# Kernel tuning notes

Measured on AMD Instinct MI355X. Metric: run time of the kernel, lower is better.

The kernel has to match this reference:

```python
import jax, jax.numpy as jnp
import numpy as np

D_MODEL = 256
D_FFN = 1024
N_LEVELS = 4
N_HEADS = 8
N_POINTS = 4
HEAD_DIM = D_MODEL // N_HEADS
SPATIAL = [(128, 128), (64, 64), (32, 32), (16, 16)]
LQ = sum(h * w for h, w in SPATIAL)  # 21760
B = 2


def setup_inputs() -> dict:
    key = jax.random.key(0)
    ks = jax.random.split(key, 24)

    def w(k, shape, s=0.02):
        return (jax.random.normal(k, shape) * s).astype(jnp.float32)

    HLP = N_HEADS * N_LEVELS * N_POINTS
    starts = np.cumsum([0] + [h * w_ for h, w_ in SPATIAL[:-1]])
    return {
        "src": jax.random.normal(ks[0], (B, LQ, D_MODEL), jnp.float32),
        "pos": 0.1 * jax.random.normal(ks[1], (B, LQ, D_MODEL), jnp.float32),
        "reference_points": jax.random.uniform(ks[2], (B, LQ, N_LEVELS, 2), jnp.float32),
        "W_off": w(ks[3], (D_MODEL, HLP * 2)),
        "b_off": w(ks[4], (HLP * 2,), 0.5),
        "W_attn": w(ks[5], (D_MODEL, HLP)),
        "b_attn": jnp.zeros((HLP,), jnp.float32),
        "W_val": w(ks[6], (D_MODEL, D_MODEL)),
        "b_val": jnp.zeros((D_MODEL,), jnp.float32),
        "W_out": w(ks[7], (D_MODEL, D_MODEL)),
        "b_out": jnp.zeros((D_MODEL,), jnp.float32),
        "ln1_g": jnp.ones((D_MODEL,), jnp.float32),
        "ln1_b": jnp.zeros((D_MODEL,), jnp.float32),
        "W1": w(ks[8], (D_MODEL, D_FFN)),
        "b1": jnp.zeros((D_FFN,), jnp.float32),
        "W2": w(ks[9], (D_FFN, D_MODEL)),
        "b2": jnp.zeros((D_MODEL,), jnp.float32),
        "ln2_g": jnp.ones((D_MODEL,), jnp.float32),
        "ln2_b": jnp.zeros((D_MODEL,), jnp.float32),
        "spatial_shapes": np.array(SPATIAL, np.int32),
        "level_start_index": np.array(starts, np.int32),
    }


def _layernorm(x, g, b):
    mu = x.mean(-1, keepdims=True)
    var = ((x - mu) ** 2).mean(-1, keepdims=True)
    return (x - mu) * jax.lax.rsqrt(var + 1e-5) * g + b


def _bilinear_sample(v, x, y, H, W):
    # v: [N, H, W, D]; x, y: [N, Lq, P] pixel coords (align_corners=False, zero pad)
    x0f = jnp.floor(x)
    y0f = jnp.floor(y)
    x0 = x0f.astype(jnp.int32)
    y0 = y0f.astype(jnp.int32)
    wx1 = x - x0f
    wy1 = y - y0f
    wx0 = 1.0 - wx1
    wy0 = 1.0 - wy1
    vf = v.reshape(v.shape[0], H * W, v.shape[-1])

    def gather(xi, yi, wt):
        valid = (xi >= 0) & (xi < W) & (yi >= 0) & (yi < H)
        idx = jnp.clip(yi, 0, H - 1) * W + jnp.clip(xi, 0, W - 1)
        g = jnp.take_along_axis(vf, idx.reshape(idx.shape[0], -1)[..., None], axis=1)
        g = g.reshape(*xi.shape, vf.shape[-1])
        return g * (wt * valid.astype(wt.dtype))[..., None]

    return (gather(x0, y0, wx0 * wy0) + gather(x0 + 1, y0, wx1 * wy0)
            + gather(x0, y0 + 1, wx0 * wy1) + gather(x0 + 1, y0 + 1, wx1 * wy1))


def _ms_deform_attn(query, src, reference_points, W_off, b_off, W_attn, b_attn,
                    W_val, b_val, W_out, b_out, spatial_shapes):
    Bq, Lq, _ = query.shape
    ss = np.asarray(spatial_shapes)
    value = (src @ W_val + b_val).reshape(Bq, Lq, N_HEADS, HEAD_DIM)
    off = (query @ W_off + b_off).reshape(Bq, Lq, N_HEADS, N_LEVELS, N_POINTS, 2)
    attn = (query @ W_attn + b_attn).reshape(Bq, Lq, N_HEADS, N_LEVELS * N_POINTS)
    attn = jax.nn.softmax(attn, axis=-1).reshape(Bq, Lq, N_HEADS, N_LEVELS, N_POINTS)
    # offset normalizer = (W, H) per level
    normalizer = jnp.asarray(ss[:, ::-1].astype(np.float32))  # [L, 2]
    loc = reference_points[:, :, None, :, None, :] + off / normalizer[None, None, None, :, None, :]
    # loc: [B, Lq, M, L, P, 2] normalized in [0,1]
    out = jnp.zeros((Bq, N_HEADS, Lq, HEAD_DIM), query.dtype)
    start = 0
    for lvl in range(N_LEVELS):
        H, W = int(ss[lvl, 0]), int(ss[lvl, 1])
        v = value[:, start:start + H * W]                                 # [B, HW, M, D]
        v = v.transpose(0, 2, 1, 3).reshape(Bq * N_HEADS, H, W, HEAD_DIM)
        l = loc[:, :, :, lvl]                                             # [B, Lq, M, P, 2]
        x = (l[..., 0] * W - 0.5).transpose(0, 2, 1, 3).reshape(Bq * N_HEADS, Lq, N_POINTS)
        y = (l[..., 1] * H - 0.5).transpose(0, 2, 1, 3).reshape(Bq * N_HEADS, Lq, N_POINTS)
        sampled = _bilinear_sample(v, x, y, H, W)                         # [BM, Lq, P, D]
        wgt = attn[:, :, :, lvl].transpose(0, 2, 1, 3).reshape(Bq * N_HEADS, Lq, N_POINTS)
        out = out + (sampled * wgt[..., None]).sum(2).reshape(Bq, N_HEADS, Lq, HEAD_DIM)
        start += H * W
    out = out.transpose(0, 2, 1, 3).reshape(Bq, Lq, D_MODEL)
    return out @ W_out + b_out


def reference(src, pos, reference_points, W_off, b_off, W_attn, b_attn, W_val, b_val,
              W_out, b_out, ln1_g, ln1_b, W1, b1, W2, b2, ln2_g, ln2_b,
              spatial_shapes, level_start_index):
    query = src + pos
    src2 = _ms_deform_attn(query, src, reference_points, W_off, b_off, W_attn, b_attn,
                           W_val, b_val, W_out, b_out, spatial_shapes)
    h = _layernorm(src + src2, ln1_g, ln1_b)
    ffn = jax.nn.relu(h @ W1 + b1) @ W2 + b2
    return _layernorm(h + ffn, ln2_g, ln2_b)
```

## Files before the change

kernel.cpp:

```cpp
#include <hip/hip_runtime.h>

typedef __bf16 bf16x8 __attribute__((ext_vector_type(8)));
typedef float f32x4 __attribute__((ext_vector_type(4)));

static constexpr int TOKS = 43520;
static constexpr int LQN  = 21760;

__device__ __forceinline__ unsigned short f2bf(float f) {
  union { float f; unsigned u; } v; v.f = f;
  return (unsigned short)((v.u + 0x7fffu + ((v.u >> 16) & 1u)) >> 16);
}
__device__ __forceinline__ float bf2f(unsigned short b) {
  union { unsigned u; float f; } v; v.u = ((unsigned)b) << 16; return v.f;
}

__global__ __launch_bounds__(256) void prewt_kernel(
    const float* __restrict__ src, const float* __restrict__ pos,
    unsigned short* __restrict__ srcb, unsigned short* __restrict__ qb,
    const float* __restrict__ W_val, const float* __restrict__ W_off,
    const float* __restrict__ W_attn, const float* __restrict__ W_out,
    const float* __restrict__ W1, const float* __restrict__ W2,
    const float* __restrict__ b_off, const float* __restrict__ b_attn,
    unsigned short* __restrict__ Wt_val, unsigned short* __restrict__ Wt_oa,
    unsigned short* __restrict__ Wt_out,
    unsigned short* __restrict__ Wt_1, unsigned short* __restrict__ Wt_2,
    float* __restrict__ b_oa) {
  const int bid = blockIdx.x;
  if (bid < 10880) {
    int i = bid * 256 + threadIdx.x;
    float4 s = ((const float4*)src)[i], p = ((const float4*)pos)[i];
    ((ushort4*)srcb)[i] = make_ushort4(f2bf(s.x), f2bf(s.y), f2bf(s.z), f2bf(s.w));
    ((ushort4*)qb)[i]   = make_ushort4(f2bf(s.x + p.x), f2bf(s.y + p.y),
                                       f2bf(s.z + p.z), f2bf(s.w + p.w));
    return;
  }
  int gid = (bid - 10880) * 256 + threadIdx.x;
  if (gid >= 754048) return;
  if (gid >= 753664) {
    int i = gid - 753664;
    b_oa[i] = (i < 256) ? b_off[i] : b_attn[i - 256];
    return;
  }
  const float* W; unsigned short* Wt; int idx, K, nsh;
  if (gid < 65536)       { W = W_val;  Wt = Wt_val;          idx = gid;          K = 256;  nsh = 8;  }
  else if (gid < 131072) { W = W_off;  Wt = Wt_oa;           idx = gid - 65536;  K = 256;  nsh = 8;  }
  else if (gid < 163840) { W = W_attn; Wt = Wt_oa + 65536;   idx = gid - 131072; K = 256;  nsh = 7;  }
  else if (gid < 229376) { W = W_out;  Wt = Wt_out;          idx = gid - 163840; K = 256;  nsh = 8;  }
  else if (gid < 491520) { W = W1;     Wt = Wt_1;            idx = gid - 229376; K = 256;  nsh = 10; }
  else                   { W = W2;     Wt = Wt_2;            idx = gid - 491520; K = 1024; nsh = 8;  }
  int k = idx >> nsh, n = idx & ((1 << nsh) - 1);
  Wt[n * K + k] = f2bf(W[idx]);
}

template <int K, int OUTOP>
__device__ __forceinline__ void gemm_body(unsigned short* __restrict__ As,
                                          unsigned short* __restrict__ Bs,
                                          const unsigned short* __restrict__ A,
                                          const unsigned short* __restrict__ Bt,
                                          const float* __restrict__ bias,
                                          const unsigned short* __restrict__ res,
                                          unsigned short* __restrict__ Cp,
                                          int N, int bm, int bn) {
  const int t = threadIdx.x;
  const int wave = t >> 6, lane = t & 63;
  const int wm = (wave & 1) << 6, wn = (wave >> 1) << 6;
  const int lr = lane & 15, lq = lane >> 4;
  const int row0 = t >> 2, cb0 = (t & 3) << 3;
  f32x4 acc[4][4] = {};
  const unsigned short* ga = A  + (size_t)(bm * 128 + row0) * K + cb0;
  const unsigned short* gb = Bt + (size_t)(bn * 128 + row0) * K + cb0;
  const size_t gs = (size_t)64 * K;
  uint4 pa0 = *(const uint4*)ga;
  uint4 pa1 = *(const uint4*)(ga + gs);
  uint4 pb0 = *(const uint4*)gb;
  uint4 pb1 = *(const uint4*)(gb + gs);
  int p = 0;
#pragma unroll 1
  for (int k0 = 0; k0 < K; k0 += 32) {
    unsigned short* Ab = As + p * 5120;
    unsigned short* Bb = Bs + p * 5120;
    *(uint4*)&Ab[row0 * 40 + cb0] = pa0;
    *(uint4*)&Ab[(row0 + 64) * 40 + cb0] = pa1;
    *(uint4*)&Bb[row0 * 40 + cb0] = pb0;
    *(uint4*)&Bb[(row0 + 64) * 40 + cb0] = pb1;
    __syncthreads();
    if (k0 + 32 < K) {
      pa0 = *(const uint4*)(ga + k0 + 32);
      pa1 = *(const uint4*)(ga + gs + k0 + 32);
      pb0 = *(const uint4*)(gb + k0 + 32);
      pb1 = *(const uint4*)(gb + gs + k0 + 32);
    }
    bf16x8 af[4], bfr[4];
#pragma unroll
    for (int i = 0; i < 4; i++) af[i] = *(const bf16x8*)&Ab[(wm + i * 16 + lr) * 40 + lq * 8];
#pragma unroll
    for (int j = 0; j < 4; j++) bfr[j] = *(const bf16x8*)&Bb[(wn + j * 16 + lr) * 40 + lq * 8];
#pragma unroll
    for (int i = 0; i < 4; i++)
#pragma unroll
      for (int j = 0; j < 4; j++)
        acc[i][j] = __builtin_amdgcn_mfma_f32_16x16x32_bf16(af[i], bfr[j], acc[i][j], 0, 0, 0);
    p ^= 1;
  }
  const int rb = bm * 128 + wm + lq * 4;
  const int cbase = bn * 128 + wn + lr;
#pragma unroll
  for (int j = 0; j < 4; j++) {
    const int col = cbase + j * 16;
    const float bv = bias[col];
#pragma unroll
    for (int i = 0; i < 4; i++) {
#pragma unroll
      for (int r = 0; r < 4; r++) {
        float v = acc[i][j][r] + bv;
        size_t o = (size_t)(rb + i * 16 + r) * N + col;
        if (OUTOP == 1) Cp[o] = f2bf(v);
        else if (OUTOP == 2) Cp[o] = f2bf(fmaxf(v, 0.f));
        else Cp[o] = f2bf(v + bf2f(res[o]));
      }
    }
  }
}

__global__ __launch_bounds__(256) void proj_kernel(
    const unsigned short* __restrict__ srcb, const unsigned short* __restrict__ qb,
    const unsigned short* __restrict__ Wt_val, const unsigned short* __restrict__ Wt_oa,
    const float* __restrict__ b_val, const float* __restrict__ b_oa,
    unsigned short* __restrict__ valb, unsigned short* __restrict__ oab) {
  __shared__ unsigned short As[2 * 5120];
  __shared__ unsigned short Bs[2 * 5120];
  const int bn = blockIdx.y;
  if (bn < 2)
    gemm_body<256, 1>(As, Bs, srcb, Wt_val, b_val, nullptr, valb, 256, blockIdx.x, bn);
  else
    gemm_body<256, 1>(As, Bs, qb, Wt_oa, b_oa, nullptr, oab, 384, blockIdx.x, bn - 2);
}

__global__ __launch_bounds__(256, 2) void fused_tail_kernel(
    const unsigned short* __restrict__ attn,
    const unsigned short* __restrict__ Wot,
    const float* __restrict__ b_out,
    const unsigned short* __restrict__ srcres,
    const float* __restrict__ g1, const float* __restrict__ be1,
    const unsigned short* __restrict__ W1t,
    const unsigned short* __restrict__ W2t,
    const float* __restrict__ b1, const float* __restrict__ b2,
    const float* __restrict__ g2, const float* __restrict__ be2,
    float* __restrict__ out) {
  __shared__ unsigned short Ah[64 * 264];
  __shared__ unsigned short Hc[64 * 136];
  __shared__ float red[2][4][64];
  const int t = threadIdx.x;
  const int w = t >> 6, lane = t & 63;
  const int lr = lane & 15, lq = lane >> 4;
  const size_t rowbase = (size_t)blockIdx.x * 64;

  {
    const uint4* gsrc = (const uint4*)(attn + rowbase * 256);
#pragma unroll
    for (int u = 0; u < 8; u++) {
      const int idx = u * 256 + t;
      const int row = idx >> 5, c8 = idx & 31;
      *(uint4*)&Ah[row * 264 + c8 * 8] = gsrc[idx];
    }
  }
  __syncthreads();

  f32x4 acc0[4][4] = {};
  {
    const size_t wb = (size_t)(w * 64 + lr) * 256;
    bf16x8 pf0 = *(const bf16x8*)&Wot[wb + lq * 8];
    bf16x8 pf1 = *(const bf16x8*)&Wot[wb + 16 * 256 + lq * 8];
    bf16x8 pf2 = *(const bf16x8*)&Wot[wb + 32 * 256 + lq * 8];
    bf16x8 pf3 = *(const bf16x8*)&Wot[wb + 48 * 256 + lq * 8];
#pragma unroll 1
    for (int ks = 0; ks < 8; ks++) {
      const int k0 = ks * 32;
      bf16x8 c0 = pf0, c1 = pf1, c2 = pf2, c3 = pf3;
      if (ks < 7) {
        pf0 = *(const bf16x8*)&Wot[wb + k0 + 32 + lq * 8];
        pf1 = *(const bf16x8*)&Wot[wb + 16 * 256 + k0 + 32 + lq * 8];
        pf2 = *(const bf16x8*)&Wot[wb + 32 * 256 + k0 + 32 + lq * 8];
        pf3 = *(const bf16x8*)&Wot[wb + 48 * 256 + k0 + 32 + lq * 8];
      }
      bf16x8 af[4];
#pragma unroll
      for (int i = 0; i < 4; i++)
        af[i] = *(const bf16x8*)&Ah[(i * 16 + lr) * 264 + k0 + lq * 8];
#pragma unroll
      for (int i = 0; i < 4; i++) {
        acc0[i][0] = __builtin_amdgcn_mfma_f32_16x16x32_bf16(af[i], c0, acc0[i][0], 0, 0, 0);
        acc0[i][1] = __builtin_amdgcn_mfma_f32_16x16x32_bf16(af[i], c1, acc0[i][1], 0, 0, 0);
        acc0[i][2] = __builtin_amdgcn_mfma_f32_16x16x32_bf16(af[i], c2, acc0[i][2], 0, 0, 0);
        acc0[i][3] = __builtin_amdgcn_mfma_f32_16x16x32_bf16(af[i], c3, acc0[i][3], 0, 0, 0);
      }
    }
  }
  {
    float vsum[4][4], vsq[4][4];
#pragma unroll
    for (int i = 0; i < 4; i++)
#pragma unroll
      for (int r = 0; r < 4; r++) { vsum[i][r] = 0.f; vsq[i][r] = 0.f; }
#pragma unroll
    for (int j = 0; j < 4; j++) {
      const int col = w * 64 + j * 16 + lr;
      const float bv = b_out[col];
#pragma unroll
      for (int i = 0; i < 4; i++)
#pragma unroll
        for (int r = 0; r < 4; r++) {
          const int row = i * 16 + lq * 4 + r;
          float v = acc0[i][j][r] + bv + bf2f(srcres[(rowbase + row) * 256 + col]);
          acc0[i][j][r] = v;
          vsum[i][r] += v;
          vsq[i][r]  += v * v;
        }
    }
#pragma unroll
    for (int m = 1; m <= 8; m <<= 1)
#pragma unroll
      for (int i = 0; i < 4; i++)
#pragma unroll
        for (int r = 0; r < 4; r++) {
          vsum[i][r] += __shfl_xor(vsum[i][r], m, 64);
          vsq[i][r]  += __shfl_xor(vsq[i][r],  m, 64);
        }
    if (lr == 0) {
#pragma unroll
      for (int i = 0; i < 4; i++)
#pragma unroll
        for (int r = 0; r < 4; r++) {
          const int row = i * 16 + lq * 4 + r;
          red[0][w][row] = vsum[i][r];
          red[1][w][row] = vsq[i][r];
        }
    }
    __syncthreads();
    float mu[4][4], rstd[4][4];
#pragma unroll
    for (int i = 0; i < 4; i++)
#pragma unroll
      for (int r = 0; r < 4; r++) {
        const int row = i * 16 + lq * 4 + r;
        const float ts = red[0][0][row] + red[0][1][row] + red[0][2][row] + red[0][3][row];
        const float tq = red[1][0][row] + red[1][1][row] + red[1][2][row] + red[1][3][row];
        const float m_ = ts * (1.f / 256.f);
        mu[i][r] = m_;
        rstd[i][r] = rsqrtf(tq * (1.f / 256.f) - m_ * m_ + 1e-5f);
      }
#pragma unroll
    for (int j = 0; j < 4; j++) {
      const int col = w * 64 + j * 16 + lr;
      const float gg = g1[col], bb = be1[col];
#pragma unroll
      for (int i = 0; i < 4; i++)
#pragma unroll
        for (int r = 0; r < 4; r++) {
          const int row = i * 16 + lq * 4 + r;
          const float y = (acc0[i][j][r] - mu[i][r]) * rstd[i][r] * gg + bb;
          Ah[row * 264 + col] = f2bf(y);
        }
    }
  }
  __syncthreads();

  f32x4 acc2[4][4] = {};
  const int c1base = w * 32;
#pragma unroll 1
  for (int c2 = 0; c2 < 8; c2++) {
    f32x4 acc1[4][2] = {};
    const size_t w1r0 = (size_t)(c2 * 128 + c1base + lr) * 256;
    const size_t w1r1 = (size_t)(c2 * 128 + c1base + 16 + lr) * 256;
    bf16x8 bfn0 = *(const bf16x8*)&W1t[w1r0 + lq * 8];
    bf16x8 bfn1 = *(const bf16x8*)&W1t[w1r1 + lq * 8];
#pragma unroll 1
    for (int ks = 0; ks < 8; ks++) {
      const int k0 = ks * 32;
      bf16x8 b0 = bfn0, b1v = bfn1;
      if (ks < 7) {
        bfn0 = *(const bf16x8*)&W1t[w1r0 + k0 + 32 + lq * 8];
        bfn1 = *(const bf16x8*)&W1t[w1r1 + k0 + 32 + lq * 8];
      }
      bf16x8 af[4];
#pragma unroll
      for (int i = 0; i < 4; i++)
        af[i] = *(const bf16x8*)&Ah[(i * 16 + lr) * 264 + k0 + lq * 8];
#pragma unroll
      for (int i = 0; i < 4; i++) {
        acc1[i][0] = __builtin_amdgcn_mfma_f32_16x16x32_bf16(af[i], b0,  acc1[i][0], 0, 0, 0);
        acc1[i][1] = __builtin_amdgcn_mfma_f32_16x16x32_bf16(af[i], b1v, acc1[i][1], 0, 0, 0);
      }
    }
    __syncthreads();
#pragma unroll
    for (int j = 0; j < 2; j++) {
      const int colc = c1base + j * 16 + lr;
      const float bv = b1[c2 * 128 + colc];
#pragma unroll
      for (int i = 0; i < 4; i++)
#pragma unroll
        for (int r = 0; r < 4; r++)
          Hc[(i * 16 + lq * 4 + r) * 136 + colc] = f2bf(fmaxf(acc1[i][j][r] + bv, 0.f));
    }
    __syncthreads();
    const size_t w2base = (size_t)(w * 64 + lr) * 1024 + c2 * 128;
    bf16x8 cfn0 = *(const bf16x8*)&W2t[w2base + lq * 8];
    bf16x8 cfn1 = *(const bf16x8*)&W2t[w2base + 16 * 1024 + lq * 8];
    bf16x8 cfn2 = *(const bf16x8*)&W2t[w2base + 32 * 1024 + lq * 8];
    bf16x8 cfn3 = *(const bf16x8*)&W2t[w2base + 48 * 1024 + lq * 8];
#pragma unroll 1
    for (int ks = 0; ks < 4; ks++) {
      const int k2 = ks * 32;
      bf16x8 c0 = cfn0, c1 = cfn1, c2v = cfn2, c3 = cfn3;
      if (ks < 3) {
        cfn0 = *(const bf16x8*)&W2t[w2base + k2 + 32 + lq * 8];
        cfn1 = *(const bf16x8*)&W2t[w2base + 16 * 1024 + k2 + 32 + lq * 8];
        cfn2 = *(const bf16x8*)&W2t[w2base + 32 * 1024 + k2 + 32 + lq * 8];
        cfn3 = *(const bf16x8*)&W2t[w2base + 48 * 1024 + k2 + 32 + lq * 8];
      }
      bf16x8 af2[4];
#pragma unroll
      for (int i = 0; i < 4; i++)
        af2[i] = *(const bf16x8*)&Hc[(i * 16 + lr) * 136 + k2 + lq * 8];
#pragma unroll
      for (int i = 0; i < 4; i++) {
        acc2[i][0] = __builtin_amdgcn_mfma_f32_16x16x32_bf16(af2[i], c0,  acc2[i][0], 0, 0, 0);
        acc2[i][1] = __builtin_amdgcn_mfma_f32_16x16x32_bf16(af2[i], c1,  acc2[i][1], 0, 0, 0);
        acc2[i][2] = __builtin_amdgcn_mfma_f32_16x16x32_bf16(af2[i], c2v, acc2[i][2], 0, 0, 0);
        acc2[i][3] = __builtin_amdgcn_mfma_f32_16x16x32_bf16(af2[i], c3,  acc2[i][3], 0, 0, 0);
      }
    }
  }
  float vsum[4][4], vsq[4][4];
#pragma unroll
  for (int i = 0; i < 4; i++)
#pragma unroll
    for (int r = 0; r < 4; r++) { vsum[i][r] = 0.f; vsq[i][r] = 0.f; }
#pragma unroll
  for (int j = 0; j < 4; j++) {
    const int col = w * 64 + j * 16 + lr;
    const float bv = b2[col];
#pragma unroll
    for (int i = 0; i < 4; i++)
#pragma unroll
      for (int r = 0; r < 4; r++) {
        const int row = i * 16 + lq * 4 + r;
        float v = acc2[i][j][r] + bv + bf2f(Ah[row * 264 + col]);
        acc2[i][j][r] = v;
        vsum[i][r] += v;
        vsq[i][r]  += v * v;
      }
  }
#pragma unroll
  for (int m = 1; m <= 8; m <<= 1)
#pragma unroll
    for (int i = 0; i < 4; i++)
#pragma unroll
      for (int r = 0; r < 4; r++) {
        vsum[i][r] += __shfl_xor(vsum[i][r], m, 64);
        vsq[i][r]  += __shfl_xor(vsq[i][r],  m, 64);
      }
  __syncthreads();
  if (lr == 0) {
#pragma unroll
    for (int i = 0; i < 4; i++)
#pragma unroll
      for (int r = 0; r < 4; r++) {
        const int row = i * 16 + lq * 4 + r;
        red[0][w][row] = vsum[i][r];
        red[1][w][row] = vsq[i][r];
      }
  }
  __syncthreads();
  float mu[4][4], rstd[4][4];
#pragma unroll
  for (int i = 0; i < 4; i++)
#pragma unroll
    for (int r = 0; r < 4; r++) {
      const int row = i * 16 + lq * 4 + r;
      const float ts = red[0][0][row] + red[0][1][row] + red[0][2][row] + red[0][3][row];
      const float tq = red[1][0][row] + red[1][1][row] + red[1][2][row] + red[1][3][row];
      const float m_ = ts * (1.f / 256.f);
      mu[i][r] = m_;
      rstd[i][r] = rsqrtf(tq * (1.f / 256.f) - m_ * m_ + 1e-5f);
    }
#pragma unroll
  for (int j = 0; j < 4; j++) {
    const int col = w * 64 + j * 16 + lr;
    const float gg = g2[col], bb = be2[col];
#pragma unroll
    for (int i = 0; i < 4; i++)
#pragma unroll
      for (int r = 0; r < 4; r++) {
        const int row = i * 16 + lq * 4 + r;
        out[(rowbase + row) * 256 + col] = (acc2[i][j][r] - mu[i][r]) * rstd[i][r] * gg + bb;
      }
  }
}

__device__ __forceinline__ void fma8(uint4 v, float w, float* a) {
  const unsigned uu[4] = {v.x, v.y, v.z, v.w};
#pragma unroll
  for (int i = 0; i < 4; i++) {
    union { unsigned u; float f; } lo, hi;
    lo.u = uu[i] << 16;
    hi.u = uu[i] & 0xffff0000u;
    a[2 * i]     += w * lo.f;
    a[2 * i + 1] += w * hi.f;
  }
}

__global__ __launch_bounds__(256) void deform_kernel(const unsigned short* __restrict__ valb,
                                                     const unsigned short* __restrict__ oab,
                                                     const float* __restrict__ refp,
                                                     unsigned short* __restrict__ outb) {
  __shared__ float4 sW[8][8][17];
  __shared__ int4   sI[8][8][17];
  const int t = threadIdx.x;
  const int bid = blockIdx.x;
  const int nb = (bid & 7) * 680 + (bid >> 3);
  const int tok0 = nb * 8;

  {
    const int g = t >> 5, h = (t >> 2) & 7, l = t & 3;
    const int tok = tok0 + g;
    const unsigned short* lg = oab + (size_t)tok * 384 + 256 + h * 16;
    uint4 lv0 = ((const uint4*)lg)[0];
    uint4 lv1 = ((const uint4*)lg)[1];
    const unsigned lw[8] = {lv0.x, lv0.y, lv0.z, lv0.w, lv1.x, lv1.y, lv1.z, lv1.w};
    float w[16];
#pragma unroll
    for (int i = 0; i < 8; i++) {
      union { unsigned u; float f; } lo, hi;
      lo.u = lw[i] << 16; hi.u = lw[i] & 0xffff0000u;
      w[2 * i] = lo.f; w[2 * i + 1] = hi.f;
    }
    float mx = -1e30f;
#pragma unroll
    for (int i = 0; i < 16; i++) mx = fmaxf(mx, w[i]);
    float s = 0.f;
#pragma unroll
    for (int i = 0; i < 16; i++) { w[i] = __expf(w[i] - mx); s += w[i]; }
    const float inv = 1.f / s;
    uint4 ov = *(const uint4*)(oab + (size_t)tok * 384 + h * 32 + l * 8);
    const unsigned owv[4] = {ov.x, ov.y, ov.z, ov.w};
    float off[8];
#pragma unroll
    for (int i = 0; i < 4; i++) {
      union { unsigned u; float f; } lo, hi;
      lo.u = owv[i] << 16; hi.u = owv[i] & 0xffff0000u;
      off[2 * i] = lo.f; off[2 * i + 1] = hi.f;
    }
    const float* rp = refp + (size_t)tok * 8 + l * 2;
    const int S = 128 >> l;
    const float Sf = (float)S;
    const float rx = rp[0] * Sf - 0.5f;
    const float ry = rp[1] * Sf - 0.5f;
#pragma unroll
    for (int p = 0; p < 4; p++) {
      const int idx = l * 4 + p;
      const float x = rx + off[p * 2 + 0];
      const float y = ry + off[p * 2 + 1];
      const float aw = w[idx] * inv;
      const float x0f = floorf(x), y0f = floorf(y);
      const int x0 = (int)x0f, y0 = (int)y0f;
      const float fx = x - x0f, fy = y - y0f;
      const bool xin0 = (x0 >= 0) & (x0 < S), xin1 = (x0 + 1 >= 0) & (x0 + 1 < S);
      const bool yin0 = (y0 >= 0) & (y0 < S), yin1 = (y0 + 1 >= 0) & (y0 + 1 < S);
      const int xc0 = min(max(x0, 0), S - 1), xc1 = min(max(x0 + 1, 0), S - 1);
      const int yc0 = min(max(y0, 0), S - 1), yc1 = min(max(y0 + 1, 0), S - 1);
      sW[g][h][idx] = make_float4(aw * (1.f - fx) * (1.f - fy) * (float)(xin0 & yin0),
                                  aw * fx * (1.f - fy)         * (float)(xin1 & yin0),
                                  aw * (1.f - fx) * fy         * (float)(xin0 & yin1),
                                  aw * fx * fy                 * (float)(xin1 & yin1));
      sI[g][h][idx] = make_int4((yc0 * S + xc0) << 9, (yc0 * S + xc1) << 9,
                                (yc1 * S + xc0) << 9, (yc1 * S + xc1) << 9);
    }
  }
  __syncthreads();

  const int g = t >> 5, h = (t >> 2) & 7, dc = t & 3;
  const int tok = tok0 + g;
  const int b = tok / LQN;
  float acc[8] = {0.f, 0.f, 0.f, 0.f, 0.f, 0.f, 0.f, 0.f};
  const int ST[4] = {0, 16384, 20480, 21504};
#pragma unroll
  for (int l = 0; l < 4; l++) {
    const char* vbc = (const char*)(valb + ((size_t)(b * LQN + ST[l])) * 256 + h * 32 + dc * 8);
#pragma unroll
    for (int p = 0; p < 4; p++) {
      float4 W4 = sW[g][h][l * 4 + p];
      int4   I4 = sI[g][h][l * 4 + p];
      uint4 v00 = *(const uint4*)(vbc + I4.x);
      uint4 v10 = *(const uint4*)(vbc + I4.y);
      uint4 v01 = *(const uint4*)(vbc + I4.z);
      uint4 v11 = *(const uint4*)(vbc + I4.w);
      fma8(v00, W4.x, acc);
      fma8(v10, W4.y, acc);
      fma8(v01, W4.z, acc);
      fma8(v11, W4.w, acc);
    }
  }
  unsigned o[4];
#pragma unroll
  for (int i = 0; i < 4; i++)
    o[i] = (unsigned)f2bf(acc[2 * i]) | ((unsigned)f2bf(acc[2 * i + 1]) << 16);
  *(uint4*)(outb + (size_t)tok * 256 + h * 32 + dc * 8) = make_uint4(o[0], o[1], o[2], o[3]);
}

extern "C" void kernel_launch(void* const* d_in, const int* in_sizes, int n_in,
                              void* d_out, int out_size, void* d_ws, size_t ws_size,
                              hipStream_t stream) {
  (void)in_sizes; (void)n_in; (void)out_size; (void)ws_size;
  const float* src    = (const float*)d_in[0];
  const float* pos    = (const float*)d_in[1];
  const float* refp   = (const float*)d_in[2];
  const float* W_off  = (const float*)d_in[3];
  const float* b_off  = (const float*)d_in[4];
  const float* W_attn = (const float*)d_in[5];
  const float* b_attn = (const float*)d_in[6];
  const float* W_val  = (const float*)d_in[7];
  const float* b_val  = (const float*)d_in[8];
  const float* W_out  = (const float*)d_in[9];
  const float* b_out  = (const float*)d_in[10];
  const float* ln1_g  = (const float*)d_in[11];
  const float* ln1_b  = (const float*)d_in[12];
  const float* W1     = (const float*)d_in[13];
  const float* b1     = (const float*)d_in[14];
  const float* W2     = (const float*)d_in[15];
  const float* b2     = (const float*)d_in[16];
  const float* ln2_g  = (const float*)d_in[17];
  const float* ln2_b  = (const float*)d_in[18];

  char* ws = (char*)d_ws;
  unsigned short* Wt_val = (unsigned short*)ws;
  unsigned short* Wt_oa  = Wt_val + 65536;
  unsigned short* Wt_out = Wt_oa + 98304;
  unsigned short* Wt_1   = Wt_out + 65536;
  unsigned short* Wt_2   = Wt_1 + 262144;
  float*          b_oa   = (float*)(Wt_2 + 262144);
  const size_t WPOOL = 2u * 1024 * 1024;

  const size_t SZ_bf = (size_t)TOKS * 256 * 2;
  const size_t SZ_oa = (size_t)TOKS * 384 * 2;

  unsigned short* srcb = (unsigned short*)(ws + WPOOL);
  unsigned short* qb   = (unsigned short*)(ws + WPOOL + SZ_bf);
  unsigned short* valb = (unsigned short*)(ws + WPOOL + 2 * SZ_bf);
  unsigned short* oab  = (unsigned short*)(ws + WPOOL + 3 * SZ_bf);
  unsigned short* attnoutb = qb;

  prewt_kernel<<<13826, 256, 0, stream>>>(src, pos, srcb, qb,
                                          W_val, W_off, W_attn, W_out, W1, W2, b_off, b_attn,
                                          Wt_val, Wt_oa, Wt_out, Wt_1, Wt_2, b_oa);

  proj_kernel<<<dim3(340, 5), 256, 0, stream>>>(srcb, qb, Wt_val, Wt_oa, b_val, b_oa,
                                                valb, oab);

  deform_kernel<<<TOKS / 8, 256, 0, stream>>>(valb, oab, refp, attnoutb);

  fused_tail_kernel<<<680, 256, 0, stream>>>(attnoutb, Wt_out, b_out, srcb, ln1_g, ln1_b,
                                             Wt_1, Wt_2, b1, b2, ln2_g, ln2_b,
                                             (float*)d_out);
}
```

Baseline: 432.0 us.

## Tile weight transposes via shared memory, deepen weight prefetch, pack deform FMAs

The weight transpose/convert now runs per 32x32 tile through shared memory, so global reads and writes are coalesced instead of strided scalar stores, and it needs far fewer blocks. The fused tail kernel's GEMM loops are fully unrolled with deeper register prefetch of weight fragments (2 to 4 steps ahead), and launch bounds are raised to 3 blocks per SM. The deform sampling accumulation uses packed float2 vector FMAs. Deeper prefetch and higher occupancy compete for registers, which may force spills.

```diff
diff --git a/kernel.cpp b/kernel.cpp
--- a/kernel.cpp
+++ b/kernel.cpp
@@ -2,6 +2,7 @@
 
 typedef __bf16 bf16x8 __attribute__((ext_vector_type(8)));
 typedef float f32x4 __attribute__((ext_vector_type(4)));
+typedef float f32x2 __attribute__((ext_vector_type(2)));
 
 static constexpr int TOKS = 43520;
 static constexpr int LQN  = 21760;
@@ -26,30 +27,45 @@
     unsigned short* __restrict__ Wt_1, unsigned short* __restrict__ Wt_2,
     float* __restrict__ b_oa) {
   const int bid = blockIdx.x;
+  const int t = threadIdx.x;
   if (bid < 10880) {
-    int i = bid * 256 + threadIdx.x;
+    int i = bid * 256 + t;
     float4 s = ((const float4*)src)[i], p = ((const float4*)pos)[i];
     ((ushort4*)srcb)[i] = make_ushort4(f2bf(s.x), f2bf(s.y), f2bf(s.z), f2bf(s.w));
     ((ushort4*)qb)[i]   = make_ushort4(f2bf(s.x + p.x), f2bf(s.y + p.y),
                                        f2bf(s.z + p.z), f2bf(s.w + p.w));
     return;
   }
-  int gid = (bid - 10880) * 256 + threadIdx.x;
-  if (gid >= 754048) return;
-  if (gid >= 753664) {
-    int i = gid - 753664;
-    b_oa[i] = (i < 256) ? b_off[i] : b_attn[i - 256];
+  if (bid == 11616) {
+    b_oa[t] = (t < 256) ? b_off[t] : 0.f;
+    if (t >= 256) return;
+    if (t < 128) b_oa[256 + t] = b_attn[t];
     return;
   }
-  const float* W; unsigned short* Wt; int idx, K, nsh;
-  if (gid < 65536)       { W = W_val;  Wt = Wt_val;          idx = gid;          K = 256;  nsh = 8;  }
-  else if (gid < 131072) { W = W_off;  Wt = Wt_oa;           idx = gid - 65536;  K = 256;  nsh = 8;  }
-  else if (gid < 163840) { W = W_attn; Wt = Wt_oa + 65536;   idx = gid - 131072; K = 256;  nsh = 7;  }
-  else if (gid < 229376) { W = W_out;  Wt = Wt_out;          idx = gid - 163840; K = 256;  nsh = 8;  }
-  else if (gid < 491520) { W = W1;     Wt = Wt_1;            idx = gid - 229376; K = 256;  nsh = 10; }
-  else                   { W = W2;     Wt = Wt_2;            idx = gid - 491520; K = 1024; nsh = 8;  }
-  int k = idx >> nsh, n = idx & ((1 << nsh) - 1);
-  Wt[n * K + k] = f2bf(W[idx]);
+  int tid = bid - 10880;
+  const float* W; unsigned short* Wt; int Kd, Nd, nshn;
+  if (tid < 64)        {            W = W_val;  Wt = Wt_val;         Kd = 256;  Nd = 256;  nshn = 3; }
+  else if (tid < 128)  { tid -= 64; W = W_off;  Wt = Wt_oa;          Kd = 256;  Nd = 256;  nshn = 3; }
+  else if (tid < 160)  { tid -= 128;W = W_attn; Wt = Wt_oa + 65536;  Kd = 256;  Nd = 128;  nshn = 2; }
+  else if (tid < 224)  { tid -= 160;W = W_out;  Wt = Wt_out;         Kd = 256;  Nd = 256;  nshn = 3; }
+  else if (tid < 480)  { tid -= 224;W = W1;     Wt = Wt_1;           Kd = 256;  Nd = 1024; nshn = 5; }
+  else                 { tid -= 480;W = W2;     Wt = Wt_2;           Kd = 1024; Nd = 256;  nshn = 3; }
+  const int k0 = (tid >> nshn) * 32;
+  const int n0 = (tid & ((1 << nshn) - 1)) * 32;
+  __shared__ float tileT[32][33];
+  {
+    const int kl = t >> 3, nc = (t & 7) * 4;
+    float4 v = *(const float4*)&W[(size_t)(k0 + kl) * Nd + n0 + nc];
+    tileT[nc + 0][kl] = v.x; tileT[nc + 1][kl] = v.y;
+    tileT[nc + 2][kl] = v.z; tileT[nc + 3][kl] = v.w;
+  }
+  __syncthreads();
+  {
+    const int nl = t >> 3, kc = (t & 7) * 4;
+    ushort4 o = make_ushort4(f2bf(tileT[nl][kc + 0]), f2bf(tileT[nl][kc + 1]),
+                             f2bf(tileT[nl][kc + 2]), f2bf(tileT[nl][kc + 3]));
+    *(ushort4*)&Wt[(size_t)(n0 + nl) * Kd + k0 + kc] = o;
+  }
 }
 
 template <int K, int OUTOP>
@@ -136,7 +152,7 @@
     gemm_body<256, 1>(As, Bs, qb, Wt_oa, b_oa, nullptr, oab, 384, blockIdx.x, bn - 2);
 }
 
-__global__ __launch_bounds__(256, 2) void fused_tail_kernel(
+__global__ __launch_bounds__(256, 3) void fused_tail_kernel(
     const unsigned short* __restrict__ attn,
     const unsigned short* __restrict__ Wot,
     const float* __restrict__ b_out,
@@ -168,25 +184,26 @@
 
   f32x4 acc0[4][4] = {};
   {
-    const size_t wb = (size_t)(w * 64 + lr) * 256;
-    bf16x8 pf0 = *(const bf16x8*)&Wot[wb + lq * 8];
-    bf16x8 pf1 = *(const bf16x8*)&Wot[wb + 16 * 256 + lq * 8];
-    bf16x8 pf2 = *(const bf16x8*)&Wot[wb + 32 * 256 + lq * 8];
-    bf16x8 pf3 = *(const bf16x8*)&Wot[wb + 48 * 256 + lq * 8];
-#pragma unroll 1
+    const size_t wb = (size_t)(w * 64 + lr) * 256 + lq * 8;
+    bf16x8 wf0[2][4];
+#pragma unroll
+    for (int d = 0; d < 2; d++)
+#pragma unroll
+      for (int j = 0; j < 4; j++)
+        wf0[d][j] = *(const bf16x8*)&Wot[wb + (size_t)j * 4096 + d * 32];
+#pragma unroll
     for (int ks = 0; ks < 8; ks++) {
-      const int k0 = ks * 32;
-      bf16x8 c0 = pf0, c1 = pf1, c2 = pf2, c3 = pf3;
-      if (ks < 7) {
-        pf0 = *(const bf16x8*)&Wot[wb + k0 + 32 + lq * 8];
-        pf1 = *(const bf16x8*)&Wot[wb + 16 * 256 + k0 + 32 + lq * 8];
-        pf2 = *(const bf16x8*)&Wot[wb + 32 * 256 + k0 + 32 + lq * 8];
-        pf3 = *(const bf16x8*)&Wot[wb + 48 * 256 + k0 + 32 + lq * 8];
+      bf16x8 c0 = wf0[ks & 1][0], c1 = wf0[ks & 1][1];
+      bf16x8 c2 = wf0[ks & 1][2], c3 = wf0[ks & 1][3];
+      if (ks + 2 < 8) {
+#pragma unroll
+        for (int j = 0; j < 4; j++)
+          wf0[ks & 1][j] = *(const bf16x8*)&Wot[wb + (size_t)j * 4096 + (ks + 2) * 32];
       }
       bf16x8 af[4];
 #pragma unroll
       for (int i = 0; i < 4; i++)
-        af[i] = *(const bf16x8*)&Ah[(i * 16 + lr) * 264 + k0 + lq * 8];
+        af[i] = *(const bf16x8*)&Ah[(i * 16 + lr) * 264 + ks * 32 + lq * 8];
 #pragma unroll
       for (int i = 0; i < 4; i++) {
         acc0[i][0] = __builtin_amdgcn_mfma_f32_16x16x32_bf16(af[i], c0, acc0[i][0], 0, 0, 0);
@@ -270,22 +287,25 @@
 #pragma unroll 1
   for (int c2 = 0; c2 < 8; c2++) {
     f32x4 acc1[4][2] = {};
-    const size_t w1r0 = (size_t)(c2 * 128 + c1base + lr) * 256;
-    const size_t w1r1 = (size_t)(c2 * 128 + c1base + 16 + lr) * 256;
-    bf16x8 bfn0 = *(const bf16x8*)&W1t[w1r0 + lq * 8];
-    bf16x8 bfn1 = *(const bf16x8*)&W1t[w1r1 + lq * 8];
-#pragma unroll 1
+    const size_t w1r0 = (size_t)(c2 * 128 + c1base + lr) * 256 + lq * 8;
+    const size_t w1r1 = w1r0 + (size_t)16 * 256;
+    bf16x8 wf[4][2];
+#pragma unroll
+    for (int d = 0; d < 4; d++) {
+      wf[d][0] = *(const bf16x8*)&W1t[w1r0 + d * 32];
+      wf[d][1] = *(const bf16x8*)&W1t[w1r1 + d * 32];
+    }
+#pragma unroll
     for (int ks = 0; ks < 8; ks++) {
-      const int k0 = ks * 32;
-      bf16x8 b0 = bfn0, b1v = bfn1;
-      if (ks < 7) {
-        bfn0 = *(const bf16x8*)&W1t[w1r0 + k0 + 32 + lq * 8];
-        bfn1 = *(const bf16x8*)&W1t[w1r1 + k0 + 32 + lq * 8];
+      bf16x8 b0 = wf[ks & 3][0], b1v = wf[ks & 3][1];
+      if (ks + 4 < 8) {
+        wf[ks & 3][0] = *(const bf16x8*)&W1t[w1r0 + (ks + 4) * 32];
+        wf[ks & 3][1] = *(const bf16x8*)&W1t[w1r1 + (ks + 4) * 32];
       }
       bf16x8 af[4];
 #pragma unroll
       for (int i = 0; i < 4; i++)
-        af[i] = *(const bf16x8*)&Ah[(i * 16 + lr) * 264 + k0 + lq * 8];
+        af[i] = *(const bf16x8*)&Ah[(i * 16 + lr) * 264 + ks * 32 + lq * 8];
 #pragma unroll
       for (int i = 0; i < 4; i++) {
         acc1[i][0] = __builtin_amdgcn_mfma_f32_16x16x32_bf16(af[i], b0,  acc1[i][0], 0, 0, 0);
@@ -304,30 +324,31 @@
           Hc[(i * 16 + lq * 4 + r) * 136 + colc] = f2bf(fmaxf(acc1[i][j][r] + bv, 0.f));
     }
     __syncthreads();
-    const size_t w2base = (size_t)(w * 64 + lr) * 1024 + c2 * 128;
-    bf16x8 cfn0 = *(const bf16x8*)&W2t[w2base + lq * 8];
-    bf16x8 cfn1 = *(const bf16x8*)&W2t[w2base + 16 * 1024 + lq * 8];
-    bf16x8 cfn2 = *(const bf16x8*)&W2t[w2base + 32 * 1024 + lq * 8];
-    bf16x8 cfn3 = *(const bf16x8*)&W2t[w2base + 48 * 1024 + lq * 8];
-#pragma unroll 1
+    const size_t w2b = (size_t)(w * 64 + lr) * 1024 + c2 * 128 + lq * 8;
+    bf16x8 wg[2][4];
+#pragma unroll
+    for (int d = 0; d < 2; d++)
+#pragma unroll
+      for (int j = 0; j < 4; j++)
+        wg[d][j] = *(const bf16x8*)&W2t[w2b + (size_t)j * 16384 + d * 32];
+#pragma unroll
     for (int ks = 0; ks < 4; ks++) {
-      const int k2 = ks * 32;
-      bf16x8 c0 = cfn0, c1 = cfn1, c2v = cfn2, c3 = cfn3;
-      if (ks < 3) {
-        cfn0 = *(const bf16x8*)&W2t[w2base + k2 + 32 + lq * 8];
-        cfn1 = *(const bf16x8*)&W2t[w2base + 16 * 1024 + k2 + 32 + lq * 8];
-        cfn2 = *(const bf16x8*)&W2t[w2base + 32 * 1024 + k2 + 32 + lq * 8];
-        cfn3 = *(const bf16x8*)&W2t[w2base + 48 * 1024 + k2 + 32 + lq * 8];
+      bf16x8 c0 = wg[ks & 1][0], c1 = wg[ks & 1][1];
+      bf16x8 cc2 = wg[ks & 1][2], c3 = wg[ks & 1][3];
+      if (ks + 2 < 4) {
+#pragma unroll
+        for (int j = 0; j < 4; j++)
+          wg[ks & 1][j] = *(const bf16x8*)&W2t[w2b + (size_t)j * 16384 + (ks + 2) * 32];
       }
       bf16x8 af2[4];
 #pragma unroll
       for (int i = 0; i < 4; i++)
-        af2[i] = *(const bf16x8*)&Hc[(i * 16 + lr) * 136 + k2 + lq * 8];
+        af2[i] = *(const bf16x8*)&Hc[(i * 16 + lr) * 136 + ks * 32 + lq * 8];
 #pragma unroll
       for (int i = 0; i < 4; i++) {
         acc2[i][0] = __builtin_amdgcn_mfma_f32_16x16x32_bf16(af2[i], c0,  acc2[i][0], 0, 0, 0);
         acc2[i][1] = __builtin_amdgcn_mfma_f32_16x16x32_bf16(af2[i], c1,  acc2[i][1], 0, 0, 0);
-        acc2[i][2] = __builtin_amdgcn_mfma_f32_16x16x32_bf16(af2[i], c2v, acc2[i][2], 0, 0, 0);
+        acc2[i][2] = __builtin_amdgcn_mfma_f32_16x16x32_bf16(af2[i], cc2, acc2[i][2], 0, 0, 0);
         acc2[i][3] = __builtin_amdgcn_mfma_f32_16x16x32_bf16(af2[i], c3,  acc2[i][3], 0, 0, 0);
       }
     }
@@ -399,15 +420,16 @@
   }
 }
 
-__device__ __forceinline__ void fma8(uint4 v, float w, float* a) {
+__device__ __forceinline__ void fma8(uint4 v, float w, f32x2* a) {
   const unsigned uu[4] = {v.x, v.y, v.z, v.w};
+  const f32x2 w2 = {w, w};
 #pragma unroll
   for (int i = 0; i < 4; i++) {
     union { unsigned u; float f; } lo, hi;
     lo.u = uu[i] << 16;
     hi.u = uu[i] & 0xffff0000u;
-    a[2 * i]     += w * lo.f;
-    a[2 * i + 1] += w * hi.f;
+    f32x2 val = {lo.f, hi.f};
+    a[i] += w2 * val;
   }
 }
 
@@ -483,7 +505,7 @@
   const int g = t >> 5, h = (t >> 2) & 7, dc = t & 3;
   const int tok = tok0 + g;
   const int b = tok / LQN;
-  float acc[8] = {0.f, 0.f, 0.f, 0.f, 0.f, 0.f, 0.f, 0.f};
+  f32x2 acc[4] = {};
   const int ST[4] = {0, 16384, 20480, 21504};
 #pragma unroll
   for (int l = 0; l < 4; l++) {
@@ -505,7 +527,7 @@
   unsigned o[4];
 #pragma unroll
   for (int i = 0; i < 4; i++)
-    o[i] = (unsigned)f2bf(acc[2 * i]) | ((unsigned)f2bf(acc[2 * i + 1]) << 16);
+    o[i] = (unsigned)f2bf(acc[i].x) | ((unsigned)f2bf(acc[i].y) << 16);
   *(uint4*)(outb + (size_t)tok * 256 + h * 32 + dc * 8) = make_uint4(o[0], o[1], o[2], o[3]);
 }
 
@@ -551,7 +573,7 @@
   unsigned short* oab  = (unsigned short*)(ws + WPOOL + 3 * SZ_bf);
   unsigned short* attnoutb = qb;
 
-  prewt_kernel<<<13826, 256, 0, stream>>>(src, pos, srcb, qb,
+  prewt_kernel<<<11617, 256, 0, stream>>>(src, pos, srcb, qb,
                                           W_val, W_off, W_attn, W_out, W1, W2, b_off, b_attn,
                                           Wt_val, Wt_oa, Wt_out, Wt_1, Wt_2, b_oa);
 
```

After: 429.7 us. No clear change (-0.5%).
